# Kernel optimization log

Hardware: AMD Instinct MI355X
Metric: run time of the kernel (lower is better)

Reference implementation:

```python
import jax, jax.numpy as jnp
import numpy as np

NUM_EMBEDDINGS = 8192
EMBEDDING_DIM = 256
COMMITMENT_COST = 0.25


def setup_inputs() -> dict:
    key = jax.random.key(0)
    k1, k2 = jax.random.split(key)
    z = jax.random.normal(k1, (32, EMBEDDING_DIM, 32, 32), dtype=jnp.float32)
    embedding = jax.random.normal(k2, (EMBEDDING_DIM, NUM_EMBEDDINGS), dtype=jnp.float32)
    return {"z": z, "embedding": embedding}


def reference(z, embedding):
    # z: [B, D, H, W]; embedding: [D, K]
    B, D, H, W = z.shape
    z_perm = jnp.transpose(z, (0, 2, 3, 1))          # [B, H, W, D]
    flat_z = z_perm.reshape(-1, D)                    # [N, D]
    # squared euclidean distances: ||z||^2 - 2 z.e + ||e||^2  -> [N, K]
    distances = (
        jnp.sum(flat_z * flat_z, axis=1, keepdims=True)
        - 2.0 * (flat_z @ embedding)
        + jnp.sum(embedding * embedding, axis=0, keepdims=True)
    )
    encoding_indices = jnp.argmin(distances, axis=1)  # [N]
    # gather codebook rows (same math as one-hot @ embedding.T)
    quantized = jnp.take(embedding.T, encoding_indices, axis=0)  # [N, D]
    quantized = quantized.reshape(z_perm.shape)       # [B, H, W, D]
    quantized = jnp.transpose(quantized, (0, 3, 1, 2))  # [B, D, H, W]

    e_latent_loss = jnp.mean((jax.lax.stop_gradient(quantized) - z) ** 2)
    q_latent_loss = jnp.mean((quantized - jax.lax.stop_gradient(z)) ** 2)
    loss = q_latent_loss + COMMITMENT_COST * e_latent_loss

    # straight-through estimator
    quantized_st = z + jax.lax.stop_gradient(quantized - z)
    return quantized_st, loss
```

## Files before the change

kernel.cpp:

```cpp
#include <hip/hip_runtime.h>

typedef unsigned int u32;
typedef unsigned short u16;
typedef __attribute__((ext_vector_type(8))) short bf16x8;
typedef __attribute__((ext_vector_type(4))) float f32x4;

#define KN 8192
#define DD 256
#define HW 1024
#define NP 32768
#define SPLITS 2
#define KSPLIT 4096
#define PXT 128
#define NTT 128

__device__ __forceinline__ u16 rne_bf16(float x) {
    u32 u = __float_as_uint(x);
    return (u16)((u + 0x7FFF + ((u >> 16) & 1)) >> 16);
}

__device__ __forceinline__ void glds16(const void* g, void* ldsbase) {
    __builtin_amdgcn_global_load_lds((const __attribute__((address_space(1))) u32*)g,
                                     (__attribute__((address_space(3))) u32*)ldsbase, 16, 0, 0);
}

__global__ void prep_kernel(const float* __restrict__ e, const float* __restrict__ z,
                            u16* __restrict__ eT, float* __restrict__ eTf,
                            float* __restrict__ e2f, u16* __restrict__ A) {
    const int t = threadIdx.x;
    const int bid = blockIdx.x;
    if (bid < 32) {
        int k = bid * 256 + t;
        float acc = 0.f;
#pragma unroll 8
        for (int d = 0; d < DD; ++d) {
            float v = e[(size_t)d * KN + k];
            acc = fmaf(v, v, acc);
        }
        e2f[k] = acc;
    } else if (bid < 544) {
        __shared__ float tt[64][65];
        const int b2 = bid - 32;
        const int kt = b2 & 127;
        const int dt = b2 >> 7;
        const float* ep = e + (size_t)(dt * 64) * KN + kt * 64;
        {
            int k = t & 63, d0 = t >> 6;
#pragma unroll
            for (int j = 0; j < 16; ++j) tt[d0 + j * 4][k] = ep[(size_t)(d0 + j * 4) * KN + k];
        }
        __syncthreads();
        int k = t >> 2, c0 = (t & 3) * 16;
        u16 hi[16];
        float fv[16];
#pragma unroll
        for (int j = 0; j < 16; ++j) {
            float v = tt[c0 + j][k];
            fv[j] = v;
            hi[j] = rne_bf16(v);
        }
        u16* rowp = eT + (size_t)(kt * 64 + k) * 256 + dt * 64 + c0;
        *(uint4*)(rowp) = *(uint4*)(hi);
        *(uint4*)(rowp + 8) = *(uint4*)(hi + 8);
        float* rowpf = eTf + (size_t)(kt * 64 + k) * 256 + dt * 64 + c0;
#pragma unroll
        for (int j = 0; j < 4; ++j) *(float4*)(rowpf + j * 4) = *(float4*)(fv + j * 4);
    } else {
        __shared__ float tt[64][65];
        const int b3 = bid - 544;
        const int pt = b3 & 15;
        const int dt = (b3 >> 4) & 3;
        const int b  = b3 >> 6;
        const float* zp = z + (size_t)b * (DD * HW) + (size_t)(dt * 64) * HW + pt * 64;
        {
            int p = t & 63, d0 = t >> 6;
#pragma unroll
            for (int j = 0; j < 16; ++j) tt[d0 + j * 4][p] = zp[(size_t)(d0 + j * 4) * HW + p];
        }
        __syncthreads();
        int p = t >> 2, c0 = (t & 3) * 16;
        int n = b * HW + pt * 64 + p;
        u16 hi[16];
#pragma unroll
        for (int j = 0; j < 16; ++j) hi[j] = rne_bf16(tt[c0 + j][p]);
        u16* rowp = A + (size_t)n * 256 + dt * 64 + c0;
        *(uint4*)(rowp) = *(uint4*)(hi);
        *(uint4*)(rowp + 8) = *(uint4*)(hi + 8);
    }
}

__launch_bounds__(256, 2)
__global__ void argmin_mfma_kernel(const u16* __restrict__ A,
                                   const u16* __restrict__ eT,
                                   const float* __restrict__ e2f,
                                   int* __restrict__ keys) {
    __shared__ u16 Ast[4][PXT * 64];
    __shared__ u16 Bst[NTT * 64];

    const int t = threadIdx.x;
    const int w = t >> 6;
    const int l = t & 63;
    const int split = blockIdx.x & 1;
    const int pxt   = blockIdx.x >> 1;
    const int px0 = pxt * PXT;
    const int kb0 = split * KSPLIT;

    const int swz  = (l & 7) ^ ((l >> 3) & 7);
    const int srow = l >> 3;
    const int fr = l & 15;
    const int g  = l >> 4;

#pragma unroll
    for (int c = 0; c < 4; ++c)
#pragma unroll
        for (int i = 0; i < 4; ++i) {
            int r0 = w * 32 + i * 8;
            const u16* gp = A + (size_t)(px0 + r0 + srow) * 256 + c * 64 + swz * 8;
            glds16(gp, &Ast[c][r0 * 64]);
        }

    int b1[8], b2[8];
#pragma unroll
    for (int i = 0; i < 8; ++i) { b1[i] = 0x7FFFFFFF; b2[i] = 0x7FFFFFFF; }

    for (int nt = 0; nt < KSPLIT / NTT; ++nt) {
        const int n0 = kb0 + nt * NTT;
        f32x4 acc[2][8];
#pragma unroll
        for (int mi = 0; mi < 2; ++mi)
#pragma unroll
            for (int ni = 0; ni < 8; ++ni) acc[mi][ni] = (f32x4){0.f, 0.f, 0.f, 0.f};

        for (int kit = 0; kit < 4; ++kit) {
            __syncthreads();
#pragma unroll
            for (int i = 0; i < 4; ++i) {
                int r0 = w * 32 + i * 8;
                const u16* gp = eT + (size_t)(n0 + r0 + srow) * 256 + kit * 64 + swz * 8;
                glds16(gp, &Bst[r0 * 64]);
            }
            __syncthreads();
#pragma unroll
            for (int kc = 0; kc < 2; ++kc) {
                bf16x8 af[2], bfr[8];
#pragma unroll
                for (int mi = 0; mi < 2; ++mi) {
                    int row = w * 32 + mi * 16 + fr;
                    int slt = (kc * 4 + g) ^ (row & 7);
                    af[mi] = *(const bf16x8*)&Ast[kit][row * 64 + slt * 8];
                }
#pragma unroll
                for (int ni = 0; ni < 8; ++ni) {
                    int row = ni * 16 + fr;
                    int slt = (kc * 4 + g) ^ (row & 7);
                    bfr[ni] = *(const bf16x8*)&Bst[row * 64 + slt * 8];
                }
#pragma unroll
                for (int mi = 0; mi < 2; ++mi)
#pragma unroll
                    for (int ni = 0; ni < 8; ++ni)
                        acc[mi][ni] = __builtin_amdgcn_mfma_f32_16x16x32_bf16(
                            af[mi], bfr[ni], acc[mi][ni], 0, 0, 0);
            }
        }

        float e2c[8];
        int   kc8[8];
#pragma unroll
        for (int ni = 0; ni < 8; ++ni) {
            kc8[ni] = n0 + ni * 16 + fr;
            e2c[ni] = e2f[kc8[ni]] * 256.f;
        }
#pragma unroll
        for (int mi = 0; mi < 2; ++mi)
#pragma unroll
            for (int r = 0; r < 4; ++r) {
                int ky[8];
#pragma unroll
                for (int ni = 0; ni < 8; ++ni) {
                    float d = fmaf(acc[mi][ni][r], -512.f, e2c[ni]);
                    ky[ni] = (int)d * 8192 + kc8[ni];
                }
                int m0 = min(min(ky[0], ky[1]), ky[2]);
                int m1 = min(min(ky[3], ky[4]), ky[5]);
                int m2 = min(min(ky[6], ky[7]), m0);
                int kmin = min(m1, m2);
                int i8 = mi * 4 + r;
                int v1 = min(b1[i8], kmin);
                int x  = max(b1[i8], kmin);
                b2[i8] = min(b2[i8], x);
                b1[i8] = v1;
            }
    }

    {
        int* k1 = keys + split * NP;
        int* k2 = keys + (2 + split) * NP;
        int* k3 = keys + (4 + split) * NP;
#pragma unroll
        for (int i = 0; i < 8; ++i) {
            int c1 = b1[i], c2 = b2[i], c3 = 0x7FFFFFFF;
#pragma unroll
            for (int m = 1; m < 16; m <<= 1) {
                int a1 = __shfl_xor(c1, m, 64);
                int a2 = __shfl_xor(c2, m, 64);
                int a3 = __shfl_xor(c3, m, 64);
                int m1 = min(c1, a1);
                int xx = max(c1, a1);
                int mn2 = min(c2, a2);
                int m2 = min(xx, mn2);
                int m3 = min(min(max(c2, a2), max(xx, mn2)), min(c3, a3));
                c1 = m1; c2 = m2; c3 = m3;
            }
            if (fr == 0) {
                int mi = i >> 2, r = i & 3;
                int row = px0 + w * 32 + mi * 16 + g * 4 + r;
                k1[row] = c1;
                k2[row] = c2;
                k3[row] = c3;
            }
        }
    }
}

__global__ void finalize_kernel(const int* __restrict__ keys,
                                const float* __restrict__ z,
                                const float* __restrict__ eTf,
                                const float* __restrict__ e2f,
                                float* __restrict__ out,
                                float* __restrict__ loss) {
    __shared__ float smem[DD * 65];
    __shared__ int   kc[384];
    __shared__ float dval[384];
    __shared__ int   kidx[64];
    const int t = threadIdx.x;
    const int n0 = blockIdx.x * 64;
    const float* zp = z + (size_t)(n0 >> 10) * (DD * HW) + (n0 & (HW - 1));

    for (int i = t; i < DD * 64; i += 256) {
        int d = i >> 6, p = i & 63;
        smem[d * 65 + p] = zp[(size_t)d * HW + p];
    }
    for (int i = t; i < 384; i += 256)
        kc[i] = keys[(i % 6) * NP + n0 + i / 6] & 8191;
    __syncthreads();

    const int l = t & 63, w = t >> 6;
    const int j = l & 15;
    const int s = l >> 4;
#pragma unroll 2
    for (int it = 0; it < 24; ++it) {
        int dot = it * 16 + w * 4 + s;
        int p = dot / 6;
        int k = kc[dot];
        const float* er = eTf + (size_t)k * 256;
        float a = 0.f;
#pragma unroll
        for (int cc = 0; cc < 16; ++cc)
            a = fmaf(smem[(cc * 16 + j) * 65 + p], er[cc * 16 + j], a);
        a += __shfl_xor(a, 1, 64);
        a += __shfl_xor(a, 2, 64);
        a += __shfl_xor(a, 4, 64);
        a += __shfl_xor(a, 8, 64);
        if (j == 0) dval[dot] = fmaf(-2.f, a, e2f[k]);
    }
    __syncthreads();
    if (t < 64) {
        float bv = dval[t * 6];
        int   bk = kc[t * 6];
#pragma unroll
        for (int c = 1; c < 6; ++c) {
            float dv = dval[t * 6 + c];
            int   kk = kc[t * 6 + c];
            if (dv < bv || (dv == bv && kk < bk)) { bv = dv; bk = kk; }
        }
        kidx[t] = bk;
    }
    __syncthreads();

    float* qt = smem;
    for (int m = 0; m < 64; ++m)
        qt[m * 257 + t] = eTf[(size_t)kidx[m] * 256 + t];
    __syncthreads();

    const int p = t & 63, q = t >> 6;
    const size_t base = (size_t)(n0 >> 10) * (DD * HW) + (n0 & (HW - 1)) + p;
    float acc = 0.f;
#pragma unroll 8
    for (int i = 0; i < 64; ++i) {
        int d = q * 64 + i;
        float ev = qt[p * 257 + d];
        float zv = z[base + (size_t)d * HW];
        out[base + (size_t)d * HW] = zv + (ev - zv);
        float df = ev - zv;
        acc = fmaf(df, df, acc);
    }
#pragma unroll
    for (int off = 32; off > 0; off >>= 1) acc += __shfl_down(acc, off, 64);
    __shared__ float part[4];
    if ((t & 63) == 0) part[t >> 6] = acc;
    __syncthreads();
    if (t == 0) {
        float s2 = (part[0] + part[1] + part[2] + part[3]) * (1.25f / 8388608.f);
        atomicAdd(loss, s2);
    }
}

__global__ void combine_kernel(const int* __restrict__ keys,
                               const float* __restrict__ z,
                               const float* __restrict__ eTf,
                               const float* __restrict__ e2f,
                               int* __restrict__ idx) {
    __shared__ float zt[DD * 65];
    __shared__ int   kc[384];
    __shared__ float dval[384];
    const int t = threadIdx.x;
    const int n0 = blockIdx.x * 64;
    const float* zp = z + (size_t)(n0 >> 10) * (DD * HW) + (n0 & (HW - 1));
    for (int i = t; i < DD * 64; i += 256) {
        int d = i >> 6, p = i & 63;
        zt[d * 65 + p] = zp[(size_t)d * HW + p];
    }
    for (int i = t; i < 384; i += 256)
        kc[i] = keys[(i % 6) * NP + n0 + i / 6] & 8191;
    __syncthreads();

    const int l = t & 63, w = t >> 6;
    const int j = l & 15;
    const int s = l >> 4;
#pragma unroll 2
    for (int it = 0; it < 24; ++it) {
        int dot = it * 16 + w * 4 + s;
        int p = dot / 6;
        int k = kc[dot];
        const float* er = eTf + (size_t)k * 256;
        float a = 0.f;
#pragma unroll
        for (int cc = 0; cc < 16; ++cc)
            a = fmaf(zt[(cc * 16 + j) * 65 + p], er[cc * 16 + j], a);
        a += __shfl_xor(a, 1, 64);
        a += __shfl_xor(a, 2, 64);
        a += __shfl_xor(a, 4, 64);
        a += __shfl_xor(a, 8, 64);
        if (j == 0) dval[dot] = fmaf(-2.f, a, e2f[k]);
    }
    __syncthreads();
    if (t < 64) {
        float bv = dval[t * 6];
        int   bk = kc[t * 6];
#pragma unroll
        for (int c = 1; c < 6; ++c) {
            float dv = dval[t * 6 + c];
            int   kk = kc[t * 6 + c];
            if (dv < bv || (dv == bv && kk < bk)) { bv = dv; bk = kk; }
        }
        idx[n0 + t] = bk;
    }
}

__global__ void gather_slow_kernel(const float* __restrict__ z,
                                   const float* __restrict__ e,
                                   const int* __restrict__ idx,
                                   float* __restrict__ out,
                                   float* __restrict__ loss) {
    const int t = threadIdx.x;
    const int n0 = blockIdx.x * 64;
    __shared__ int kidx[64];
    if (t < 64) kidx[t] = idx[n0 + t];
    __syncthreads();

    const int p = t & 63;
    const int d0 = t >> 6;
    const size_t base = (size_t)(n0 >> 10) * (DD * HW) + (n0 & (HW - 1)) + p;
    const int kk = kidx[p];

    float acc = 0.f;
    for (int d = d0; d < DD; d += 4) {
        float ev = e[(size_t)d * KN + kk];
        float zv = z[base + (size_t)d * HW];
        out[base + (size_t)d * HW] = zv + (ev - zv);
        float df = ev - zv;
        acc = fmaf(df, df, acc);
    }
#pragma unroll
    for (int off = 32; off > 0; off >>= 1) acc += __shfl_down(acc, off, 64);
    __shared__ float part[4];
    if ((t & 63) == 0) part[t >> 6] = acc;
    __syncthreads();
    if (t == 0) {
        float s = (part[0] + part[1] + part[2] + part[3]) * (1.25f / 8388608.f);
        atomicAdd(loss, s);
    }
}

extern "C" void kernel_launch(void* const* d_in, const int* in_sizes, int n_in,
                              void* d_out, int out_size, void* d_ws, size_t ws_size,
                              hipStream_t stream) {
    const float* z = (const float*)d_in[0];
    const float* e = (const float*)d_in[1];
    float* out = (float*)d_out;
    float* loss = out + (size_t)NP * DD;

    char* ob = (char*)d_out;
    char* ws = (char*)d_ws;
    u16* Acat = (u16*)ob;
    u16* eT   = (u16*)(ob + ((size_t)16 << 20));

    float* e2f = (float*)ws;
    int*   idx = (int*)(ws + (32 << 10));
    int*   keys;
    float* eTf;
    const bool fastws = ws_size >= ((size_t)10 << 20);
    if (fastws) {
        keys = (int*)(ws + (160 << 10));
        eTf  = (float*)(ws + ((size_t)1 << 20));
    } else {
        keys = (int*)(ob + ((size_t)20 << 20));
        eTf  = (float*)(ob + ((size_t)23 << 20));
    }

    prep_kernel<<<2592, 256, 0, stream>>>(e, z, eT, eTf, e2f, Acat);
    argmin_mfma_kernel<<<SPLITS * (NP / PXT), 256, 0, stream>>>(Acat, eT, e2f, keys);
    hipMemsetAsync(loss, 0, sizeof(float), stream);
    if (fastws) {
        finalize_kernel<<<NP / 64, 256, 0, stream>>>(keys, z, eTf, e2f, out, loss);
    } else {
        combine_kernel<<<NP / 64, 256, 0, stream>>>(keys, z, eTf, e2f, idx);
        gather_slow_kernel<<<NP / 64, 256, 0, stream>>>(z, e, idx, out, loss);
    }
}
```

Before: 267.7 us.

## Enlarge argmin GEMM tile to 256x256 with 8 waves and double-buffered B staging

Restructures the distance GEMM kernel to use 512-thread blocks computing a 256-pixel by 256-code tile, with each wave holding a 64x128 sub-tile. It also double-buffers the codebook slices in LDS and overlaps the next slice's global-to-LDS load with the current MFMA work, using fewer barriers and s_setprio around the MFMAs. The goal is higher arithmetic intensity and less LDS and global traffic per MFMA than the 128x128 single-buffered tile. In exchange, register pressure rises (64 accumulators plus 32 running top-2 keys per lane), LDS use is larger (about 160KB), and an extra cross-wave merge of the top-3 keys through LDS is needed.

```diff
diff --git a/kernel.cpp b/kernel.cpp
--- a/kernel.cpp
+++ b/kernel.cpp
@@ -11,8 +11,9 @@
 #define NP 32768
 #define SPLITS 2
 #define KSPLIT 4096
-#define PXT 128
-#define NTT 128
+#define BROW 256
+#define BCOL 256
+#define NTILES (KSPLIT / BCOL)
 
 __device__ __forceinline__ u16 rne_bf16(float x) {
     u32 u = __float_as_uint(x);
@@ -89,90 +90,87 @@
     }
 }
 
-__launch_bounds__(256, 2)
+
+#define STAGE_A(kit)                                                              \
+    do {                                                                          \
+        const u16* as_ = asrc + (kit) * 32;                                       \
+        glds16(as_,             &Ast[(kit) * 8192 + w * 512]);                    \
+        glds16(as_ + 128 * 256, &Ast[(kit) * 8192 + (8 + w) * 512]);              \
+    } while (0)
+
+#define STAGE_B(eoff, buf)                                                        \
+    do {                                                                          \
+        const u16* bs_ = bsrc0 + (eoff);                                          \
+        glds16(bs_,             &Bst[buf][w * 512]);                              \
+        glds16(bs_ + 128 * 256, &Bst[buf][(8 + w) * 512]);                        \
+    } while (0)
+
+#define COMPUTE_KIT(kit, first)                                                   \
+    do {                                                                          \
+        bf16x8 af[4], bfr[8];                                                     \
+        const u16* bq_ = &Bst[(kit) & 1][0];                                      \
+        _Pragma("unroll")                                                         \
+        for (int mi = 0; mi < 4; ++mi)                                            \
+            af[mi] = *(const bf16x8*)&Ast[(kit) * 8192 + aoff + mi * 512];        \
+        _Pragma("unroll")                                                         \
+        for (int ni = 0; ni < 8; ++ni)                                            \
+            bfr[ni] = *(const bf16x8*)&bq_[boff + ni * 512];                      \
+        __builtin_amdgcn_s_setprio(1);                                            \
+        _Pragma("unroll")                                                         \
+        for (int mi = 0; mi < 4; ++mi)                                            \
+            _Pragma("unroll")                                                     \
+            for (int ni = 0; ni < 8; ++ni)                                        \
+                acc[mi][ni] = __builtin_amdgcn_mfma_f32_16x16x32_bf16(            \
+                    af[mi], bfr[ni], (first) ? zacc : acc[mi][ni], 0, 0, 0);      \
+        __builtin_amdgcn_s_setprio(0);                                            \
+    } while (0)
+
+__launch_bounds__(512, 2)
 __global__ void argmin_mfma_kernel(const u16* __restrict__ A,
                                    const u16* __restrict__ eT,
                                    const float* __restrict__ e2f,
                                    int* __restrict__ keys) {
-    __shared__ u16 Ast[4][PXT * 64];
-    __shared__ u16 Bst[NTT * 64];
+    __shared__ __align__(16) u16 Ast[8 * 8192];
+    __shared__ __align__(16) u16 Bst[2][8192];
 
     const int t = threadIdx.x;
     const int w = t >> 6;
     const int l = t & 63;
+    const int wm = w & 3;
+    const int wn = w >> 2;
+    const int fr = l & 15;
+    const int g  = l >> 4;
+
     const int split = blockIdx.x & 1;
     const int pxt   = blockIdx.x >> 1;
-    const int px0 = pxt * PXT;
+    const int px0 = pxt * BROW;
     const int kb0 = split * KSPLIT;
 
-    const int swz  = (l & 7) ^ ((l >> 3) & 7);
-    const int srow = l >> 3;
-    const int fr = l & 15;
-    const int g  = l >> 4;
-
-#pragma unroll
-    for (int c = 0; c < 4; ++c)
-#pragma unroll
-        for (int i = 0; i < 4; ++i) {
-            int r0 = w * 32 + i * 8;
-            const u16* gp = A + (size_t)(px0 + r0 + srow) * 256 + c * 64 + swz * 8;
-            glds16(gp, &Ast[c][r0 * 64]);
-        }
-
-    int b1[8], b2[8];
-#pragma unroll
-    for (int i = 0; i < 8; ++i) { b1[i] = 0x7FFFFFFF; b2[i] = 0x7FFFFFFF; }
-
-    for (int nt = 0; nt < KSPLIT / NTT; ++nt) {
-        const int n0 = kb0 + nt * NTT;
-        f32x4 acc[2][8];
-#pragma unroll
-        for (int mi = 0; mi < 2; ++mi)
-#pragma unroll
-            for (int ni = 0; ni < 8; ++ni) acc[mi][ni] = (f32x4){0.f, 0.f, 0.f, 0.f};
-
-        for (int kit = 0; kit < 4; ++kit) {
-            __syncthreads();
-#pragma unroll
-            for (int i = 0; i < 4; ++i) {
-                int r0 = w * 32 + i * 8;
-                const u16* gp = eT + (size_t)(n0 + r0 + srow) * 256 + kit * 64 + swz * 8;
-                glds16(gp, &Bst[r0 * 64]);
-            }
-            __syncthreads();
-#pragma unroll
-            for (int kc = 0; kc < 2; ++kc) {
-                bf16x8 af[2], bfr[8];
-#pragma unroll
-                for (int mi = 0; mi < 2; ++mi) {
-                    int row = w * 32 + mi * 16 + fr;
-                    int slt = (kc * 4 + g) ^ (row & 7);
-                    af[mi] = *(const bf16x8*)&Ast[kit][row * 64 + slt * 8];
-                }
-#pragma unroll
-                for (int ni = 0; ni < 8; ++ni) {
-                    int row = ni * 16 + fr;
-                    int slt = (kc * 4 + g) ^ (row & 7);
-                    bfr[ni] = *(const bf16x8*)&Bst[row * 64 + slt * 8];
-                }
-#pragma unroll
-                for (int mi = 0; mi < 2; ++mi)
-#pragma unroll
-                    for (int ni = 0; ni < 8; ++ni)
-                        acc[mi][ni] = __builtin_amdgcn_mfma_f32_16x16x32_bf16(
-                            af[mi], bfr[ni], acc[mi][ni], 0, 0, 0);
-            }
-        }
-
+    const int srow = l >> 2;
+    const int ssw  = ((l & 3) ^ ((l >> 2) & 3)) * 8;
+    const u16* asrc  = A  + (size_t)(px0 + w * 16 + srow) * 256 + ssw;
+    const u16* bsrc0 = eT + (size_t)(w * 16 + srow) * 256 + ssw;
+
+    const int fsw  = (g ^ (fr & 3)) * 8;
+    const int aoff = (wm * 64 + fr) * 32 + fsw;
+    const int boff = (wn * 128 + fr) * 32 + fsw;
+
+    const f32x4 zacc = (f32x4){0.f, 0.f, 0.f, 0.f};
+    f32x4 acc[4][8];
+    int b1[16], b2[16];
+#pragma unroll
+    for (int i = 0; i < 16; ++i) { b1[i] = 0x7FFFFFFF; b2[i] = 0x7FFFFFFF; }
+
+    auto epilogue = [&](int n0) {
         float e2c[8];
         int   kc8[8];
 #pragma unroll
         for (int ni = 0; ni < 8; ++ni) {
-            kc8[ni] = n0 + ni * 16 + fr;
+            kc8[ni] = n0 + wn * 128 + ni * 16 + fr;
             e2c[ni] = e2f[kc8[ni]] * 256.f;
         }
 #pragma unroll
-        for (int mi = 0; mi < 2; ++mi)
+        for (int mi = 0; mi < 4; ++mi)
 #pragma unroll
             for (int r = 0; r < 4; ++r) {
                 int ky[8];
@@ -185,41 +183,81 @@
                 int m1 = min(min(ky[3], ky[4]), ky[5]);
                 int m2 = min(min(ky[6], ky[7]), m0);
                 int kmin = min(m1, m2);
-                int i8 = mi * 4 + r;
-                int v1 = min(b1[i8], kmin);
-                int x  = max(b1[i8], kmin);
-                b2[i8] = min(b2[i8], x);
-                b1[i8] = v1;
+                int s = mi * 4 + r;
+                int v1 = min(b1[s], kmin);
+                int x  = max(b1[s], kmin);
+                b2[s] = min(b2[s], x);
+                b1[s] = v1;
             }
-    }
-
-    {
-        int* k1 = keys + split * NP;
-        int* k2 = keys + (2 + split) * NP;
-        int* k3 = keys + (4 + split) * NP;
-#pragma unroll
-        for (int i = 0; i < 8; ++i) {
-            int c1 = b1[i], c2 = b2[i], c3 = 0x7FFFFFFF;
-#pragma unroll
-            for (int m = 1; m < 16; m <<= 1) {
-                int a1 = __shfl_xor(c1, m, 64);
-                int a2 = __shfl_xor(c2, m, 64);
-                int a3 = __shfl_xor(c3, m, 64);
-                int m1 = min(c1, a1);
-                int xx = max(c1, a1);
-                int mn2 = min(c2, a2);
-                int m2 = min(xx, mn2);
-                int m3 = min(min(max(c2, a2), max(xx, mn2)), min(c3, a3));
-                c1 = m1; c2 = m2; c3 = m3;
-            }
-            if (fr == 0) {
-                int mi = i >> 2, r = i & 3;
-                int row = px0 + w * 32 + mi * 16 + g * 4 + r;
-                k1[row] = c1;
-                k2[row] = c2;
-                k3[row] = c3;
-            }
-        }
+    };
+
+    STAGE_A(0);
+    STAGE_B((size_t)kb0 * 256, 0);
+    STAGE_A(1);
+    asm volatile("s_waitcnt vmcnt(2)" ::: "memory");
+    __builtin_amdgcn_s_barrier();
+
+#pragma unroll
+    for (int kit = 0; kit < 8; ++kit) {
+        if (kit < 7) STAGE_B((size_t)kb0 * 256 + (kit + 1) * 32, (kit + 1) & 1);
+        else         STAGE_B(((size_t)kb0 + BCOL) * 256, 0);
+        if (kit < 6) STAGE_A(kit + 2);
+        COMPUTE_KIT(kit, kit == 0);
+        if (kit < 6) { asm volatile("s_waitcnt vmcnt(2)" ::: "memory"); }
+        else         { asm volatile("s_waitcnt vmcnt(0)" ::: "memory"); }
+        __builtin_amdgcn_s_barrier();
+    }
+    epilogue(kb0);
+
+    for (int nt = 1; nt < NTILES; ++nt) {
+        const int n0 = kb0 + nt * BCOL;
+#pragma unroll
+        for (int kit = 0; kit < 8; ++kit) {
+            if (kit < 7)
+                STAGE_B((size_t)n0 * 256 + (kit + 1) * 32, (kit + 1) & 1);
+            else if (nt < NTILES - 1)
+                STAGE_B(((size_t)n0 + BCOL) * 256, 0);
+            COMPUTE_KIT(kit, kit == 0);
+            __syncthreads();
+        }
+        epilogue(n0);
+    }
+
+    int* mrg = (int*)&Bst[0][0];
+#pragma unroll
+    for (int s = 0; s < 16; ++s) {
+        int c1 = b1[s], c2 = b2[s], c3 = 0x7FFFFFFF;
+#pragma unroll
+        for (int m = 1; m < 16; m <<= 1) {
+            int a1 = __shfl_xor(c1, m, 64);
+            int a2 = __shfl_xor(c2, m, 64);
+            int a3 = __shfl_xor(c3, m, 64);
+            int m1 = min(c1, a1);
+            int xx = max(c1, a1);
+            int mn2 = min(c2, a2);
+            int m2 = min(xx, mn2);
+            int m3 = min(min(max(c2, a2), max(xx, mn2)), min(c3, a3));
+            c1 = m1; c2 = m2; c3 = m3;
+        }
+        if (fr == 0) {
+            int row = wm * 64 + (s >> 2) * 16 + g * 4 + (s & 3);
+            int o = (wn * 256 + row) * 3;
+            mrg[o] = c1; mrg[o + 1] = c2; mrg[o + 2] = c3;
+        }
+    }
+    __syncthreads();
+    if (t < 256) {
+        int a1 = mrg[t * 3], a2 = mrg[t * 3 + 1], a3 = mrg[t * 3 + 2];
+        int u1 = mrg[(256 + t) * 3], u2 = mrg[(256 + t) * 3 + 1], u3 = mrg[(256 + t) * 3 + 2];
+        int x1 = min(a1, u1), y1 = max(a1, u1);
+        int n2 = min(a2, u2), M2 = max(a2, u2);
+        int c1 = x1;
+        int c2 = min(y1, n2);
+        int c3 = min(max(y1, n2), min(M2, min(a3, u3)));
+        int row = px0 + t;
+        keys[split * NP + row]       = c1;
+        keys[(2 + split) * NP + row] = c2;
+        keys[(4 + split) * NP + row] = c3;
     }
 }
 
@@ -420,7 +458,7 @@
     }
 
     prep_kernel<<<2592, 256, 0, stream>>>(e, z, eT, eTf, e2f, Acat);
-    argmin_mfma_kernel<<<SPLITS * (NP / PXT), 256, 0, stream>>>(Acat, eT, e2f, keys);
+    argmin_mfma_kernel<<<SPLITS * (NP / BROW), 512, 0, stream>>>(Acat, eT, e2f, keys);
     hipMemsetAsync(loss, 0, sizeof(float), stream);
     if (fastws) {
         finalize_kernel<<<NP / 64, 256, 0, stream>>>(keys, z, eTf, e2f, out, loss);
```

Measured after the change: 287.4 us. +7.4%, slower.
